# Kernel tuning notes

Hardware: AMD Instinct MI355X
Metric: run time of the kernel (lower is better)

The kernel has to match this reference:

```python
import jax, jax.numpy as jnp
import numpy as np

NUM_KEYS = 100000
NUM_VALUES = 100000
KEY_SIZE = 256
VALUE_SIZE = 256
B = 4096
K = 50


def setup_inputs() -> dict:
    key = jax.random.key(0)
    k1, k2, k3, k4, k5, k6 = jax.random.split(key, 6)
    keys = jax.random.randint(k1, (B, K), 0, NUM_KEYS, dtype=jnp.int64 if jax.config.jax_enable_x64 else jnp.int32)
    values = jax.random.randint(k2, (B, K), 0, NUM_VALUES, dtype=keys.dtype)
    pair_length = jnp.maximum(jax.random.randint(k3, (B,), 0, K, dtype=keys.dtype), 1)
    query = jax.random.normal(k4, (B, KEY_SIZE), dtype=jnp.float32)
    key_table = jax.random.normal(k5, (NUM_KEYS, KEY_SIZE), dtype=jnp.float32)
    value_table = jax.random.normal(k6, (NUM_VALUES, VALUE_SIZE), dtype=jnp.float32)
    return {"keys": keys, "values": values, "pair_length": pair_length,
            "query": query, "key_table": key_table, "value_table": value_table}


def reference(keys, values, pair_length, query, key_table, value_table):
    # Gather per-example key/value embeddings: (B, K, D)
    k_emb = key_table[keys]
    v_emb = value_table[values]
    # Scores: query . key_emb -> (B, K)
    logits = jnp.einsum('bd,bkd->bk', query, k_emb)
    # Mask positions >= pair_length, then stable softmax over valid entries
    mask = jnp.arange(k_emb.shape[1])[None, :] < pair_length[:, None]
    neg_inf = jnp.finfo(logits.dtype).min
    prob = jax.nn.softmax(jnp.where(mask, logits, neg_inf), axis=1)
    # Weighted value sum -> (B, value_size)
    knowledge = jnp.einsum('bk,bkd->bd', prob, v_emb)
    return knowledge
```

## Files before the change

kernel.cpp:

```cpp
#include <hip/hip_runtime.h>
#include <math.h>

#define BATCH 4096
#define KMAX 50
#define DIM 256

__global__ __launch_bounds__(256) void kv_memory_kernel(
    const int* __restrict__ keys,
    const int* __restrict__ values,
    const int* __restrict__ pair_len,
    const float* __restrict__ query,
    const float* __restrict__ key_table,
    const float* __restrict__ value_table,
    float* __restrict__ out)
{
    const int b    = blockIdx.x;
    const int tid  = threadIdx.x;
    const int lane = tid & 63;
    const int wave = tid >> 6;

    __shared__ int   s_keys[KMAX];
    __shared__ int   s_vals[KMAX];
    __shared__ float s_logit[64];
    __shared__ float s_prob[64];
    __shared__ float4 s_acc[4][64];

    int len = pair_len[b];
    if (len < 1) len = 1;
    if (len > KMAX) len = KMAX;

    if (tid < KMAX) {
        s_keys[tid] = keys[b * KMAX + tid];
        s_vals[tid] = values[b * KMAX + tid];
    }

    const float4 q = *reinterpret_cast<const float4*>(query + (size_t)b * DIM + lane * 4);
    __syncthreads();

    for (int k = wave; k < KMAX; k += 4) {
        float lg = -INFINITY;
        if (k < len) {
            const float4 kr = *reinterpret_cast<const float4*>(
                key_table + (size_t)s_keys[k] * DIM + lane * 4);
            float p = q.x * kr.x + q.y * kr.y + q.z * kr.z + q.w * kr.w;
            #pragma unroll
            for (int off = 32; off; off >>= 1) p += __shfl_xor(p, off);
            lg = p;
        }
        if (lane == 0) s_logit[k] = lg;
    }
    __syncthreads();

    if (wave == 0) {
        float lg = (lane < len) ? s_logit[lane] : -INFINITY;
        float m = lg;
        #pragma unroll
        for (int off = 32; off; off >>= 1) m = fmaxf(m, __shfl_xor(m, off));
        float e = (lane < len) ? __expf(lg - m) : 0.0f;
        float s = e;
        #pragma unroll
        for (int off = 32; off; off >>= 1) s += __shfl_xor(s, off);
        const float inv = 1.0f / s;
        if (lane < KMAX) s_prob[lane] = e * inv;
    }
    __syncthreads();

    float4 acc = make_float4(0.f, 0.f, 0.f, 0.f);
    for (int k = wave; k < len; k += 4) {
        const float  p = s_prob[k];
        const float4 v = *reinterpret_cast<const float4*>(
            value_table + (size_t)s_vals[k] * DIM + lane * 4);
        acc.x += p * v.x;
        acc.y += p * v.y;
        acc.z += p * v.z;
        acc.w += p * v.w;
    }
    s_acc[wave][lane] = acc;
    __syncthreads();

    if (wave == 0) {
        float4 a0 = s_acc[0][lane];
        const float4 a1 = s_acc[1][lane];
        const float4 a2 = s_acc[2][lane];
        const float4 a3 = s_acc[3][lane];
        a0.x += a1.x + a2.x + a3.x;
        a0.y += a1.y + a2.y + a3.y;
        a0.z += a1.z + a2.z + a3.z;
        a0.w += a1.w + a2.w + a3.w;
        *reinterpret_cast<float4*>(out + (size_t)b * DIM + lane * 4) = a0;
    }
}

extern "C" void kernel_launch(void* const* d_in, const int* in_sizes, int n_in,
                              void* d_out, int out_size, void* d_ws, size_t ws_size,
                              hipStream_t stream) {
    const int*   keys        = (const int*)d_in[0];
    const int*   values      = (const int*)d_in[1];
    const int*   pair_len    = (const int*)d_in[2];
    const float* query       = (const float*)d_in[3];
    const float* key_table   = (const float*)d_in[4];
    const float* value_table = (const float*)d_in[5];
    float* out = (float*)d_out;

    kv_memory_kernel<<<BATCH, 256, 0, stream>>>(
        keys, values, pair_len, query, key_table, value_table, out);
}
```

Before: 39.55 us.

## Batch all key/value row gathers per wave and softmax redundantly in every wave

Fully unrolls the key and value gather loops so each wave issues all 13 row loads up front, clamping out-of-range indices to the last valid row and relying on zero weights or unused logits. This exposes more memory-level parallelism for the latency-bound random gathers. The softmax is also recomputed in every wave, with weights distributed by shuffle, which removes the shared probability array and one block barrier. In exchange it raises register pressure (13 float4 per phase) and loads duplicate rows for short pair lengths.

After: 36.64 us. 1.08x faster.

```diff
diff --git a/kernel.cpp b/kernel.cpp
--- a/kernel.cpp
+++ b/kernel.cpp
@@ -4,6 +4,7 @@
 #define BATCH 4096
 #define KMAX 50
 #define DIM 256
+#define NITER 13
 
 __global__ __launch_bounds__(256) void kv_memory_kernel(
     const int* __restrict__ keys,
@@ -19,10 +20,9 @@
     const int lane = tid & 63;
     const int wave = tid >> 6;
 
-    __shared__ int   s_keys[KMAX];
-    __shared__ int   s_vals[KMAX];
-    __shared__ float s_logit[64];
-    __shared__ float s_prob[64];
+    __shared__ int    s_keys[KMAX];
+    __shared__ int    s_vals[KMAX];
+    __shared__ float  s_logit[64];
     __shared__ float4 s_acc[4][64];
 
     int len = pair_len[b];
@@ -37,43 +37,70 @@
     const float4 q = *reinterpret_cast<const float4*>(query + (size_t)b * DIM + lane * 4);
     __syncthreads();
 
-    for (int k = wave; k < KMAX; k += 4) {
-        float lg = -INFINITY;
-        if (k < len) {
-            const float4 kr = *reinterpret_cast<const float4*>(
-                key_table + (size_t)s_keys[k] * DIM + lane * 4);
-            float p = q.x * kr.x + q.y * kr.y + q.z * kr.z + q.w * kr.w;
-            #pragma unroll
-            for (int off = 32; off; off >>= 1) p += __shfl_xor(p, off);
-            lg = p;
+    int kidx[NITER];
+    #pragma unroll
+    for (int i = 0; i < NITER; ++i) {
+        const int k  = wave + 4 * i;
+        const int kc = (k < len) ? k : (len - 1);
+        kidx[i] = s_keys[kc];
+    }
+    float4 kr[NITER];
+    #pragma unroll
+    for (int i = 0; i < NITER; ++i) {
+        kr[i] = *reinterpret_cast<const float4*>(
+            key_table + (size_t)kidx[i] * DIM + lane * 4);
+    }
+    float dot[NITER];
+    #pragma unroll
+    for (int i = 0; i < NITER; ++i) {
+        dot[i] = q.x * kr[i].x + q.y * kr[i].y + q.z * kr[i].z + q.w * kr[i].w;
+    }
+    #pragma unroll
+    for (int off = 32; off; off >>= 1) {
+        #pragma unroll
+        for (int i = 0; i < NITER; ++i) dot[i] += __shfl_xor(dot[i], off);
+    }
+    if (lane == 0) {
+        #pragma unroll
+        for (int i = 0; i < NITER; ++i) {
+            const int k = wave + 4 * i;
+            s_logit[k] = dot[i];
         }
-        if (lane == 0) s_logit[k] = lg;
     }
     __syncthreads();
 
-    if (wave == 0) {
-        float lg = (lane < len) ? s_logit[lane] : -INFINITY;
-        float m = lg;
-        #pragma unroll
-        for (int off = 32; off; off >>= 1) m = fmaxf(m, __shfl_xor(m, off));
-        float e = (lane < len) ? __expf(lg - m) : 0.0f;
-        float s = e;
-        #pragma unroll
-        for (int off = 32; off; off >>= 1) s += __shfl_xor(s, off);
-        const float inv = 1.0f / s;
-        if (lane < KMAX) s_prob[lane] = e * inv;
+    float lg = (lane < len) ? s_logit[lane] : -INFINITY;
+    float m = lg;
+    #pragma unroll
+    for (int off = 32; off; off >>= 1) m = fmaxf(m, __shfl_xor(m, off));
+    float e = (lane < len) ? __expf(lg - m) : 0.0f;
+    float s = e;
+    #pragma unroll
+    for (int off = 32; off; off >>= 1) s += __shfl_xor(s, off);
+    const float p = e * (1.0f / s);
+
+    int   vidx[NITER];
+    float w[NITER];
+    #pragma unroll
+    for (int i = 0; i < NITER; ++i) {
+        const int k  = wave + 4 * i;
+        const int kc = (k < len) ? k : (len - 1);
+        vidx[i] = s_vals[kc];
+        w[i]    = __shfl(p, (k < 63) ? k : 63);
     }
-    __syncthreads();
-
+    float4 vr[NITER];
+    #pragma unroll
+    for (int i = 0; i < NITER; ++i) {
+        vr[i] = *reinterpret_cast<const float4*>(
+            value_table + (size_t)vidx[i] * DIM + lane * 4);
+    }
     float4 acc = make_float4(0.f, 0.f, 0.f, 0.f);
-    for (int k = wave; k < len; k += 4) {
-        const float  p = s_prob[k];
-        const float4 v = *reinterpret_cast<const float4*>(
-            value_table + (size_t)s_vals[k] * DIM + lane * 4);
-        acc.x += p * v.x;
-        acc.y += p * v.y;
-        acc.z += p * v.z;
-        acc.w += p * v.w;
+    #pragma unroll
+    for (int i = 0; i < NITER; ++i) {
+        acc.x += w[i] * vr[i].x;
+        acc.y += w[i] * vr[i].y;
+        acc.z += w[i] * vr[i].z;
+        acc.w += w[i] * vr[i].w;
     }
     s_acc[wave][lane] = acc;
     __syncthreads();
```
